# Performance work log

Measured on AMD Instinct MI355X. Metric: run time of the kernel, lower is better.

Reference implementation:

```python
import jax, jax.numpy as jnp
import numpy as np

B, S, D, H, FF = 2, 2048, 1024, 16, 4096
DK = D // H
LOCAL_WINDOW, STRIDE = 128, 128
NEG = -1000000000.0
EPS = 1e-5


def _layernorm(x, g, b):
    mu = jnp.mean(x, axis=-1, keepdims=True)
    var = jnp.mean(jnp.square(x - mu), axis=-1, keepdims=True)
    return (x - mu) * jax.lax.rsqrt(var + EPS) * g + b


def _strided_mask(seq):
    # allowed(i, j): j <= i and (i-j <= local_window or (i-j) % stride == 0)
    i = jnp.arange(seq)[:, None]
    j = jnp.arange(seq)[None, :]
    d = i - j
    return (d >= 0) & ((d <= LOCAL_WINDOW) | (d % STRIDE == 0))  # [S, S] bool


def setup_inputs() -> dict:
    key = jax.random.key(0)
    ks = jax.random.split(key, 18)
    w = lambda k, shape: jax.random.normal(k, shape, jnp.float32) * 0.02
    return {
        "x": jax.random.normal(ks[0], (B, S, D), jnp.float32),
        "mask": jnp.ones((1, 1, S, S), jnp.int32),
        "Wq": w(ks[1], (D, D)), "bq": jnp.zeros((D,), jnp.float32),
        "Wk": w(ks[2], (D, D)), "bk": jnp.zeros((D,), jnp.float32),
        "Wv": w(ks[3], (D, D)), "bv": jnp.zeros((D,), jnp.float32),
        "Wo": w(ks[4], (D, D)), "bo": jnp.zeros((D,), jnp.float32),
        "W1": w(ks[5], (D, FF)), "bf1": jnp.zeros((FF,), jnp.float32),
        "W2": w(ks[6], (FF, D)), "bf2": jnp.zeros((D,), jnp.float32),
        "g1": jnp.ones((D,), jnp.float32), "bl1": jnp.zeros((D,), jnp.float32),
        "g2": jnp.ones((D,), jnp.float32), "bl2": jnp.zeros((D,), jnp.float32),
    }


def reference(x, mask, Wq, bq, Wk, bk, Wv, bv, Wo, bo,
              W1, bf1, W2, bf2, g1, bl1, g2, bl2):
    b, s, d = x.shape
    sm = _strided_mask(s)[None, None]  # [1,1,S,S]

    # pre-LN self-attention
    n = _layernorm(x, g1, bl1)
    split = lambda t: t.reshape(b, s, H, DK).transpose(0, 2, 1, 3)  # [B,H,S,DK]
    q = split(n @ Wq + bq)
    k = split(n @ Wk + bk)
    v = split(n @ Wv + bv)

    scores = jnp.einsum('bhqd,bhkd->bhqk', q, k) / jnp.sqrt(jnp.float32(DK))
    scores = jnp.where(sm, scores, NEG)          # strided/local mask
    scores = jnp.where(mask == 0, NEG, scores)   # user mask
    attn = jax.nn.softmax(scores, axis=-1)
    o = jnp.einsum('bhqk,bhkd->bhqd', attn, v)
    o = o.transpose(0, 2, 1, 3).reshape(b, s, d) @ Wo + bo
    x = x + o

    # pre-LN FFN (GELU exact, matching torch nn.GELU default)
    n2 = _layernorm(x, g2, bl2)
    ff = jax.nn.gelu(n2 @ W1 + bf1, approximate=False) @ W2 + bf2
    return x + ff
```

## Files before the change

### kernel.cpp

```cpp
#include <hip/hip_runtime.h>
#include <math.h>

typedef unsigned int u32;
typedef unsigned short u16;

#define B_  2
#define S_  2048
#define D_  1024
#define H_  16
#define DK_ 64
#define FF_ 4096
#define NEG_ -1000000000.0f

typedef __attribute__((ext_vector_type(8))) short short8;
typedef __attribute__((ext_vector_type(4))) float floatx4;
typedef __attribute__((ext_vector_type(4))) unsigned short ushort4_t;

__device__ inline u16 f2b(float f) {
    union { float f; u32 u; } v; v.f = f;
    u32 r = (v.u + 0x7fffu + ((v.u >> 16) & 1u)) >> 16;
    return (u16)r;
}
__device__ inline float b2f(u16 b) {
    union { u32 u; float f; } v; v.u = ((u32)b) << 16;
    return v.f;
}

__device__ inline void gl_lds16(const u16* g, u16* l) {
    __builtin_amdgcn_global_load_lds((const __attribute__((address_space(1))) u32*)g,
                                     (__attribute__((address_space(3))) u32*)l, 16, 0, 0);
}

__global__ void tconv4(const float* __restrict__ W0, const float* __restrict__ W1_,
                       const float* __restrict__ W2_, const float* __restrict__ W3,
                       u16* __restrict__ dstBase) {
    __shared__ float tile[32][33];
    int z = blockIdx.z;
    const float* Wm = (z == 0) ? W0 : (z == 1) ? W1_ : (z == 2) ? W2_ : W3;
    u16* Wt = dstBase + (size_t)z * 1024 * 1024;
    const int K = 1024, N = 1024;
    int n0 = blockIdx.x * 32, k0 = blockIdx.y * 32;
    int tx = threadIdx.x & 31, ty = threadIdx.x >> 5;
#pragma unroll
    for (int r = 0; r < 32; r += 8)
        tile[ty + r][tx] = Wm[(size_t)(k0 + ty + r) * N + n0 + tx];
    __syncthreads();
#pragma unroll
    for (int r = 0; r < 32; r += 8)
        Wt[(size_t)(n0 + ty + r) * K + k0 + tx] = f2b(tile[tx][ty + r]);
}

__global__ void tconv(const float* __restrict__ Wm, u16* __restrict__ Wt, int K, int N) {
    __shared__ float tile[32][33];
    int n0 = blockIdx.x * 32, k0 = blockIdx.y * 32;
    int tx = threadIdx.x & 31, ty = threadIdx.x >> 5;
#pragma unroll
    for (int r = 0; r < 32; r += 8)
        tile[ty + r][tx] = Wm[(size_t)(k0 + ty + r) * N + n0 + tx];
    __syncthreads();
#pragma unroll
    for (int r = 0; r < 32; r += 8)
        Wt[(size_t)(n0 + ty + r) * K + k0 + tx] = f2b(tile[tx][ty + r]);
}

__global__ void catbias(const float* __restrict__ bq, const float* __restrict__ bk,
                        const float* __restrict__ bv, float* __restrict__ out) {
    int i = blockIdx.x * 256 + threadIdx.x;
    float v = (i < 1024) ? bq[i] : (i < 2048) ? bk[i - 1024] : bv[i - 2048];
    out[i] = v;
}

__global__ __launch_bounds__(256)
void mask_tiles(const int* __restrict__ mask, int* __restrict__ tflag) {
    int jt = blockIdx.x, it = blockIdx.y;
    const int* base = mask + (size_t)it * 128 * S_ + jt * 128;
    int t = threadIdx.x;
    int ok = 1;
    for (int e = t; e < 128 * 32; e += 256) {
        int r = e >> 5, c4 = e & 31;
        int4 vv = *(const int4*)&base[(size_t)r * S_ + c4 * 4];
        ok &= (vv.x != 0) & (vv.y != 0) & (vv.z != 0) & (vv.w != 0);
    }
    ok = (int)__all(ok);
    __shared__ int red[4];
    if ((t & 63) == 0) red[t >> 6] = ok;
    __syncthreads();
    if (t == 0) tflag[it * 16 + jt] = red[0] & red[1] & red[2] & red[3];
}

__global__ __launch_bounds__(256)
void ln_bf16(const float* __restrict__ x, const float* __restrict__ g,
             const float* __restrict__ b, u16* __restrict__ out) {
    int row = blockIdx.x, t = threadIdx.x;
    int lane = t & 63, w = t >> 6;
    const float* xr = x + (size_t)row * D_;
    __shared__ float red[8];
    int col0 = t * 4;
    float4 xv = *(const float4*)&xr[col0];
    float v0 = xv.x, v1 = xv.y, v2 = xv.z, v3 = xv.w;
    float s = v0 + v1 + v2 + v3;
    s += __shfl_xor(s, 1); s += __shfl_xor(s, 2); s += __shfl_xor(s, 4);
    s += __shfl_xor(s, 8); s += __shfl_xor(s, 16); s += __shfl_xor(s, 32);
    if (lane == 0) red[w] = s;
    __syncthreads();
    float mu = (red[0] + red[1] + red[2] + red[3]) * (1.0f / D_);
    float d0 = v0 - mu, d1 = v1 - mu, d2 = v2 - mu, d3 = v3 - mu;
    float vs = d0 * d0 + d1 * d1 + d2 * d2 + d3 * d3;
    vs += __shfl_xor(vs, 1); vs += __shfl_xor(vs, 2); vs += __shfl_xor(vs, 4);
    vs += __shfl_xor(vs, 8); vs += __shfl_xor(vs, 16); vs += __shfl_xor(vs, 32);
    if (lane == 0) red[4 + w] = vs;
    __syncthreads();
    float rstd = rsqrtf((red[4] + red[5] + red[6] + red[7]) * (1.0f / D_) + 1e-5f);
    float4 gv = *(const float4*)&g[col0];
    float4 bv = *(const float4*)&b[col0];
    ushort4_t o;
    o[0] = f2b(d0 * rstd * gv.x + bv.x);
    o[1] = f2b(d1 * rstd * gv.y + bv.y);
    o[2] = f2b(d2 * rstd * gv.z + bv.z);
    o[3] = f2b(d3 * rstd * gv.w + bv.w);
    *(ushort4_t*)&out[(size_t)row * D_ + col0] = o;
}

__global__ __launch_bounds__(256)
void merge_ln(const u16* __restrict__ P, const float* __restrict__ x,
              const float* __restrict__ bo, const float* __restrict__ g,
              const float* __restrict__ bl, float* __restrict__ x1,
              u16* __restrict__ n2) {
    const size_t MN = (size_t)B_ * S_ * D_;
    int row = blockIdx.x, t = threadIdx.x;
    int lane = t & 63, w = t >> 6;
    size_t base = (size_t)row * D_;
    __shared__ float red[8];
    int col0 = t * 4;
    float4 xv = *(const float4*)&x[base + col0];
    float4 bv = *(const float4*)&bo[col0];
    ushort4_t p0 = *(const ushort4_t*)&P[base + col0];
    ushort4_t p1 = *(const ushort4_t*)&P[MN + base + col0];
    float v0 = xv.x + bv.x + b2f(p0[0]) + b2f(p1[0]);
    float v1 = xv.y + bv.y + b2f(p0[1]) + b2f(p1[1]);
    float v2 = xv.z + bv.z + b2f(p0[2]) + b2f(p1[2]);
    float v3 = xv.w + bv.w + b2f(p0[3]) + b2f(p1[3]);
    float s = v0 + v1 + v2 + v3;
    s += __shfl_xor(s, 1); s += __shfl_xor(s, 2); s += __shfl_xor(s, 4);
    s += __shfl_xor(s, 8); s += __shfl_xor(s, 16); s += __shfl_xor(s, 32);
    if (lane == 0) red[w] = s;
    __syncthreads();
    float mu = (red[0] + red[1] + red[2] + red[3]) * (1.0f / D_);
    float d0 = v0 - mu, d1 = v1 - mu, d2 = v2 - mu, d3 = v3 - mu;
    float vs = d0 * d0 + d1 * d1 + d2 * d2 + d3 * d3;
    vs += __shfl_xor(vs, 1); vs += __shfl_xor(vs, 2); vs += __shfl_xor(vs, 4);
    vs += __shfl_xor(vs, 8); vs += __shfl_xor(vs, 16); vs += __shfl_xor(vs, 32);
    if (lane == 0) red[4 + w] = vs;
    __syncthreads();
    float rstd = rsqrtf((red[4] + red[5] + red[6] + red[7]) * (1.0f / D_) + 1e-5f);
    float4 gv = *(const float4*)&g[col0];
    float4 blv = *(const float4*)&bl[col0];
    *(float4*)&x1[base + col0] = (float4){v0, v1, v2, v3};
    ushort4_t o;
    o[0] = f2b(d0 * rstd * gv.x + blv.x);
    o[1] = f2b(d1 * rstd * gv.y + blv.y);
    o[2] = f2b(d2 * rstd * gv.z + blv.z);
    o[3] = f2b(d3 * rstd * gv.w + blv.w);
    *(ushort4_t*)&n2[base + col0] = o;
}

#define BARR asm volatile("s_barrier" ::: "memory")

template <int EPI>
__global__ __launch_bounds__(512, 2)
void gemm8(const u16* __restrict__ A, const u16* __restrict__ Bt,
           const float* __restrict__ bias, void* __restrict__ Cv,
           int M, int N, int K, int ldA, int ldB) {
    __shared__ u16 sh2[65536];
    const int tid = threadIdx.x;
    const int lane = tid & 63, w = tid >> 6;
    const int wm = w >> 2, wn = w & 3;
    const int c = lane & 15, g = lane >> 4;
    const int cbase = c * 128 + g * 16;
    const int xo = (c & 7) << 4;

    int nMt = gridDim.x;
    int nwg = gridDim.x * gridDim.y;
    int id = blockIdx.x + nMt * blockIdx.y;
    int qq = nwg >> 3;
    int sid = (id & 7) * qq + (id >> 3);
    int m0 = (sid % nMt) * 256, n0 = (sid / nMt) * 256;
    size_t koff = (size_t)blockIdx.z * K;

    const int nT = K >> 6, nI = nT >> 1;

    const int sr = tid >> 3;
    const int sk = ((tid & 7) * 8) ^ (((tid >> 3) & 7) << 3);
    const u16* gA0 = A + (size_t)(m0 + sr) * ldA + koff + sk;
    const u16* gB0 = Bt + (size_t)(n0 + sr) * ldB + koff + sk;
    const int dst0 = w * 512;

#define STG_A(t_, h_) do { \
    const u16* s_ = gA0 + (size_t)(h_) * 128 * ldA + (t_) * 64; \
    u16* l_ = &sh2[((((t_) & 1) * 2 + (h_)) * 8192) + dst0]; \
    gl_lds16(s_, l_); \
    gl_lds16(s_ + (size_t)64 * ldA, l_ + 4096); \
} while (0)
#define STG_B(t_, h_) do { \
    const u16* s_ = gB0 + (size_t)(h_) * 128 * ldB + (t_) * 64; \
    u16* l_ = &sh2[32768 + ((((t_) & 1) * 2 + (h_)) * 8192) + dst0]; \
    gl_lds16(s_, l_); \
    gl_lds16(s_ + (size_t)64 * ldB, l_ + 4096); \
} while (0)

    short8 fa[8], fb0[4], fb1[4];
    floatx4 acc[2][2][4][2];
#pragma unroll
    for (int i = 0; i < 2; i++)
#pragma unroll
        for (int j = 0; j < 2; j++)
#pragma unroll
            for (int a = 0; a < 4; a++)
#pragma unroll
                for (int b2 = 0; b2 < 2; b2++)
                    acc[i][j][a][b2] = (floatx4){0.f, 0.f, 0.f, 0.f};

#define DS_A(d_, qr_) do { \
    int rb_ = ((d_) * 2 + wm) * 16384; \
    _Pragma("unroll") for (int a_ = 0; a_ < 4; a_++) \
    _Pragma("unroll") for (int k_ = 0; k_ < 2; k_++) { \
        int lin_ = (qr_) * 8192 + a_ * 2048 + cbase + k_ * 64; \
        fa[a_ * 2 + k_] = *(const short8*)((const char*)sh2 + rb_ + (lin_ ^ xo)); } \
} while (0)
#define DS_B(d_, qc_, fb_) do { \
    int rb_ = 65536 + ((d_) * 2 + (wn >> 1)) * 16384; \
    _Pragma("unroll") for (int b_ = 0; b_ < 2; b_++) \
    _Pragma("unroll") for (int k_ = 0; k_ < 2; k_++) { \
        int lin_ = (wn & 1) * 8192 + (qc_) * 4096 + b_ * 2048 + cbase + k_ * 64; \
        fb_[b_ * 2 + k_] = *(const short8*)((const char*)sh2 + rb_ + (lin_ ^ xo)); } \
} while (0)
#define MFMA16(qr_, qc_, fb_) do { \
    __builtin_amdgcn_s_setprio(1); \
    _Pragma("unroll") for (int a_ = 0; a_ < 4; a_++) \
    _Pragma("unroll") for (int b_ = 0; b_ < 2; b_++) \
    _Pragma("unroll") for (int k_ = 0; k_ < 2; k_++) \
        acc[qr_][qc_][a_][b_] = __builtin_amdgcn_mfma_f32_16x16x32_bf16( \
            fa[a_ * 2 + k_], fb_[b_ * 2 + k_], acc[qr_][qc_][a_][b_], 0, 0, 0); \
    __builtin_amdgcn_s_setprio(0); \
} while (0)

    STG_B(0, 0); STG_B(0, 1); STG_A(0, 0); STG_A(0, 1);
    STG_A(1, 0); STG_A(1, 1);
    asm volatile("s_waitcnt vmcnt(4)" ::: "memory");
    BARR;

    for (int it2 = 0; it2 < nI; it2++) {
        const int t1 = 2 * it2 + 1, tn0 = t1 + 1, tn1 = t1 + 2;
        DS_A(0, 0); DS_B(0, 0, fb0);
        STG_B(t1, 0);
        MFMA16(0, 0, fb0); BARR;
        DS_B(0, 1, fb1);
        STG_B(t1, 1);
        MFMA16(0, 1, fb1); BARR;
        DS_A(0, 1);
        if (tn0 < nT) STG_B(tn0, 0);
        MFMA16(1, 1, fb1); BARR;
        if (tn0 < nT) {
            STG_B(tn0, 1);
            asm volatile("s_waitcnt vmcnt(4)" ::: "memory");
        } else {
            asm volatile("s_waitcnt vmcnt(0)" ::: "memory");
        }
        MFMA16(1, 0, fb0); BARR;
        DS_A(1, 0); DS_B(1, 0, fb0);
        if (tn0 < nT) STG_A(tn0, 0);
        MFMA16(0, 0, fb0); BARR;
        DS_B(1, 1, fb1);
        if (tn0 < nT) STG_A(tn0, 1);
        MFMA16(0, 1, fb1); BARR;
        DS_A(1, 1);
        if (tn1 < nT) STG_A(tn1, 0);
        MFMA16(1, 1, fb1); BARR;
        if (tn1 < nT) STG_A(tn1, 1);
        if (it2 + 1 < nI) asm volatile("s_waitcnt vmcnt(4)" ::: "memory");
        MFMA16(1, 0, fb0); BARR;
    }

#pragma unroll
    for (int qr = 0; qr < 2; qr++)
#pragma unroll
        for (int qc = 0; qc < 2; qc++)
#pragma unroll
            for (int a = 0; a < 4; a++)
#pragma unroll
                for (int b2 = 0; b2 < 2; b2++) {
                    int mrow = m0 + wm * 128 + qr * 64 + a * 16 + g * 4;
                    int ncol = n0 + wn * 64 + qc * 32 + b2 * 16 + c;
                    float bv = (EPI == 3) ? 0.f : bias[ncol];
#pragma unroll
                    for (int r = 0; r < 4; r++) {
                        int m = mrow + r;
                        float vvv = acc[qr][qc][a][b2][r] + bv;
                        if (EPI == 0) {
                            int which = ncol >> 10, col = ncol & 1023;
                            if (which == 0) vvv *= 0.125f;
                            int bb = m >> 11, ss = m & 2047, hh = col >> 6, dk = col & 63;
                            ((u16*)Cv)[(size_t)which * ((size_t)B_ * S_ * D_) +
                                       ((((size_t)bb * H_ + hh) * S_) + ss) * DK_ + dk] = f2b(vvv);
                        } else if (EPI == 2) {
                            float u = 0.79788456080286536f * fmaf(0.044715f * vvv, vvv * vvv, vvv);
                            float th = 1.f - 2.f / (1.f + __expf(2.f * u));
                            ((u16*)Cv)[(size_t)m * N + ncol] = f2b(0.5f * vvv * (1.f + th));
                        } else {
                            ((u16*)Cv)[(size_t)blockIdx.z * M * N + (size_t)m * N + ncol] = f2b(vvv);
                        }
                    }
                }
#undef STG_A
#undef STG_B
#undef DS_A
#undef DS_B
#undef MFMA16
}

__global__ __launch_bounds__(256)
void ffn2_merge(const u16* __restrict__ P, const float* __restrict__ x1,
                const float* __restrict__ bf2, float* __restrict__ out) {
    const size_t MN = (size_t)B_ * S_ * D_;
    int e = (blockIdx.x * 256 + threadIdx.x) * 4;
    float4 xv = *(const float4*)&x1[e];
    float4 bv = *(const float4*)&bf2[e & 1023];
    float o0 = xv.x + bv.x, o1 = xv.y + bv.y, o2 = xv.z + bv.z, o3 = xv.w + bv.w;
#pragma unroll
    for (int z = 0; z < 4; z++) {
        ushort4_t pv = *(const ushort4_t*)&P[z * MN + e];
        o0 += b2f(pv[0]); o1 += b2f(pv[1]); o2 += b2f(pv[2]); o3 += b2f(pv[3]);
    }
    *(float4*)&out[e] = (float4){o0, o1, o2, o3};
}

#define MAXB_ 14
__global__ __launch_bounds__(256)
void attn4(const u16* __restrict__ q, const u16* __restrict__ k,
           const u16* __restrict__ v, const int* __restrict__ mask,
           const int* __restrict__ tileOK, u16* __restrict__ ob) {
    __shared__ u16 sh[19456];
    u16* Kw = sh;
    u16* Qs = sh + 13824;
    u16* Vh = sh + 12800;

    const int bh = blockIdx.x;
    const int i0 = (31 - blockIdx.y) * 64;
    const int b  = bh >> 4, h = bh & 15;
    const int t  = threadIdx.x;
    const int lane = t & 63, w = t >> 6;
    const int c = lane & 15, g = lane >> 4;
    const int g4 = g * 4;
    const int qloc16 = w * 16;

    const u16* qg = q + ((size_t)bh * S_ + i0) * DK_;
    const u16* kg = k + (size_t)bh * S_ * DK_;
    const u16* vg = v + (size_t)bh * S_ * DK_;

    const int wlo = (i0 >= 128) ? i0 - 128 : 0;
    const int wn  = i0 + 64 - wlo;
    const int nb  = (i0 >= 256) ? (i0 >> 7) - 1 : 0;
    const int jb0 = i0 & 127;
    const int dd0 = i0 - wlo;

    bool allOK = true;
    {
        const int* rowf = tileOK + (i0 >> 7) * 16;
        int jt0 = wlo >> 7, jt1 = (i0 + 63) >> 7;
        for (int jt = jt0; jt <= jt1; jt++) allOK &= (rowf[jt] != 0);
        for (int m = 0; m < nb; m++) allOK &= (rowf[m] != 0);
    }

    for (int e = t; e < 64 * 8; e += 256) {
        int row = e >> 3, dc = e & 7;
        *(short8*)&Qs[row * 72 + dc * 8] = *(const short8*)(qg + row * 64 + dc * 8);
    }
    for (int e = t; e < wn * 8; e += 256) {
        int row = e >> 3, dc = e & 7;
        *(short8*)&Kw[row * 72 + dc * 8] = *(const short8*)(kg + (size_t)(wlo + row) * 64 + dc * 8);
    }
    __syncthreads();

    float sbr[MAXB_];
    {
        short8 qv0 = *(const short8*)&Qs[(qloc16 + c) * 72 + g * 8];
        short8 qv1 = *(const short8*)&Qs[(qloc16 + c) * 72 + 32 + g * 8];
#pragma unroll
        for (int m = 0; m < MAXB_; m++) {
            sbr[m] = NEG_;
            if (m < nb) {
                int jrow = jb0 + (m << 7) + qloc16 + c;
                short8 kv0 = *(const short8*)(kg + (size_t)jrow * 64 + g * 8);
                short8 kv1 = *(const short8*)(kg + (size_t)jrow * 64 + 32 + g * 8);
                float p = 0.f;
#pragma unroll
                for (int i = 0; i < 8; i++) {
                    p += b2f((u16)qv0[i]) * b2f((u16)kv0[i]);
                    p += b2f((u16)qv1[i]) * b2f((u16)kv1[i]);
                }
                p += __shfl_xor(p, 16);
                p += __shfl_xor(p, 32);
                if (!allOK && mask[(size_t)(i0 + qloc16 + c) * S_ + jrow] == 0) p = NEG_;
                sbr[m] = p;
            }
        }
    }

    floatx4 sc[12];
#pragma unroll
    for (int ct = 0; ct < 12; ct++) sc[ct] = (floatx4){0.f, 0.f, 0.f, 0.f};
    {
        short8 fa0 = *(const short8*)&Qs[(qloc16 + c) * 72 + g * 8];
        short8 fa1 = *(const short8*)&Qs[(qloc16 + c) * 72 + 32 + g * 8];
#pragma unroll
        for (int ct = 0; ct < 12; ct++) {
            short8 fb0 = *(const short8*)&Kw[(ct * 16 + c) * 72 + g * 8];
            short8 fb1 = *(const short8*)&Kw[(ct * 16 + c) * 72 + 32 + g * 8];
            sc[ct] = __builtin_amdgcn_mfma_f32_16x16x32_bf16(fa0, fb0, sc[ct], 0, 0, 0);
            sc[ct] = __builtin_amdgcn_mfma_f32_16x16x32_bf16(fa1, fb1, sc[ct], 0, 0, 0);
        }
    }

#pragma unroll
    for (int ct = 0; ct < 12; ct++) {
        int cidx = ct * 16 + c;
        int j = wlo + cidx;
#pragma unroll
        for (int r = 0; r < 4; r++) {
            int qloc = qloc16 + g4 + r;
            int d = dd0 + qloc - cidx;
            bool ok = (d >= 0) && (d <= 128);
            if (ok && !allOK) ok = (mask[(size_t)(i0 + qloc) * S_ + j] != 0);
            sc[ct][r] = ok ? sc[ct][r] : NEG_;
        }
    }

    float mv[4], inv[4];
#pragma unroll
    for (int r = 0; r < 4; r++) {
        float bs[MAXB_];
#pragma unroll
        for (int m = 0; m < MAXB_; m++)
            bs[m] = (m < nb) ? __shfl(sbr[m], g4 + r, 64) : NEG_;
        float mm = -1e30f;
#pragma unroll
        for (int ct = 0; ct < 12; ct++) mm = fmaxf(mm, sc[ct][r]);
        mm = fmaxf(mm, __shfl_xor(mm, 1));
        mm = fmaxf(mm, __shfl_xor(mm, 2));
        mm = fmaxf(mm, __shfl_xor(mm, 4));
        mm = fmaxf(mm, __shfl_xor(mm, 8));
#pragma unroll
        for (int m = 0; m < MAXB_; m++)
            if (m < nb) mm = fmaxf(mm, bs[m]);
        float sum = 0.f;
#pragma unroll
        for (int ct = 0; ct < 12; ct++) {
            float e = __expf(sc[ct][r] - mm);
            sc[ct][r] = e;
            sum += e;
        }
        sum += __shfl_xor(sum, 1);
        sum += __shfl_xor(sum, 2);
        sum += __shfl_xor(sum, 4);
        sum += __shfl_xor(sum, 8);
#pragma unroll
        for (int m = 0; m < MAXB_; m++)
            if (m < nb) sum += __expf(bs[m] - mm);
        mv[r] = mm;
        inv[r] = 1.f / sum;
    }

    __syncthreads();
    u16* P = Kw;
#pragma unroll
    for (int ct = 0; ct < 12; ct++)
#pragma unroll
        for (int r = 0; r < 4; r++)
            P[(qloc16 + g4 + r) * 200 + ct * 16 + c] = f2b(sc[ct][r]);

    for (int e = t; e < 768; e += 256) {
        int dc = e / 96, jl = e - dc * 96;
        short8 val = {0, 0, 0, 0, 0, 0, 0, 0};
        if (jl < wn) val = *(const short8*)(vg + (size_t)(wlo + jl) * 64 + dc * 8);
#pragma unroll
        for (int i = 0; i < 8; i++) Vh[(dc * 8 + i) * 104 + jl] = (u16)val[i];
    }
    __syncthreads();

    floatx4 o[4];
#pragma unroll
    for (int nt = 0; nt < 4; nt++) o[nt] = (floatx4){0.f, 0.f, 0.f, 0.f};
#pragma unroll
    for (int ks = 0; ks < 3; ks++) {
        short8 pa = *(const short8*)&P[(qloc16 + c) * 200 + ks * 32 + g * 8];
#pragma unroll
        for (int nt = 0; nt < 4; nt++) {
            short8 vb = *(const short8*)&Vh[(nt * 16 + c) * 104 + ks * 32 + g * 8];
            o[nt] = __builtin_amdgcn_mfma_f32_16x16x32_bf16(pa, vb, o[nt], 0, 0, 0);
        }
    }

    if (wn > 96) {
        __syncthreads();
        for (int e = t; e < 768; e += 256) {
            int dc = e / 96, jl = e - dc * 96;
            int j2 = 96 + jl;
            short8 val = {0, 0, 0, 0, 0, 0, 0, 0};
            if (j2 < wn) val = *(const short8*)(vg + (size_t)(wlo + j2) * 64 + dc * 8);
#pragma unroll
            for (int i = 0; i < 8; i++) Vh[(dc * 8 + i) * 104 + jl] = (u16)val[i];
        }
        __syncthreads();
#pragma unroll
        for (int ks = 0; ks < 3; ks++) {
            short8 pa = *(const short8*)&P[(qloc16 + c) * 200 + 96 + ks * 32 + g * 8];
#pragma unroll
            for (int nt = 0; nt < 4; nt++) {
                short8 vb = *(const short8*)&Vh[(nt * 16 + c) * 104 + ks * 32 + g * 8];
                o[nt] = __builtin_amdgcn_mfma_f32_16x16x32_bf16(pa, vb, o[nt], 0, 0, 0);
            }
        }
    }

#pragma unroll
    for (int m = 0; m < MAXB_; m++) {
        if (m < nb) {
            int vbase = jb0 + (m << 7) + qloc16 + g4;
            u16 vv[4][4];
#pragma unroll
            for (int r = 0; r < 4; r++)
#pragma unroll
                for (int nt = 0; nt < 4; nt++)
                    vv[r][nt] = vg[(size_t)(vbase + r) * 64 + nt * 16 + c];
#pragma unroll
            for (int r = 0; r < 4; r++) {
                float bs = __shfl(sbr[m], g4 + r, 64);
                float pb = __expf(bs - mv[r]);
#pragma unroll
                for (int nt = 0; nt < 4; nt++)
                    o[nt][r] += pb * b2f(vv[r][nt]);
            }
        }
    }

#pragma unroll
    for (int nt = 0; nt < 4; nt++) {
#pragma unroll
        for (int r = 0; r < 4; r++) {
            int qi = i0 + qloc16 + g4 + r;
            ob[((size_t)b * S_ + qi) * D_ + h * 64 + nt * 16 + c] = f2b(o[nt][r] * inv[r]);
        }
    }
}

extern "C" void kernel_launch(void* const* d_in, const int* in_sizes, int n_in,
                              void* d_out, int out_size, void* d_ws, size_t ws_size,
                              hipStream_t stream) {
    const float* x    = (const float*)d_in[0];
    const int*   mask = (const int*)  d_in[1];
    const float* Wq   = (const float*)d_in[2];
    const float* bq   = (const float*)d_in[3];
    const float* Wk   = (const float*)d_in[4];
    const float* bk   = (const float*)d_in[5];
    const float* Wv   = (const float*)d_in[6];
    const float* bv   = (const float*)d_in[7];
    const float* Wo   = (const float*)d_in[8];
    const float* bo   = (const float*)d_in[9];
    const float* W1   = (const float*)d_in[10];
    const float* bf1  = (const float*)d_in[11];
    const float* W2   = (const float*)d_in[12];
    const float* bf2  = (const float*)d_in[13];
    const float* g1   = (const float*)d_in[14];
    const float* bl1  = (const float*)d_in[15];
    const float* g2   = (const float*)d_in[16];
    const float* bl2  = (const float*)d_in[17];

    char* wsb = (char*)d_ws;
    const size_t MB = 1024 * 1024;
    u16*   WtQKV  = (u16*)(wsb + 0);
    u16*   WtO    = (u16*)(wsb + 6 * MB);
    u16*   Wt1    = (u16*)(wsb + 8 * MB);
    u16*   Wt2    = (u16*)(wsb + 16 * MB);
    u16*   n1b    = (u16*)(wsb + 24 * MB);
    u16*   qkv    = (u16*)(wsb + 32 * MB);
    u16*   obb    = (u16*)(wsb + 56 * MB);
    float* x1     = (float*)(wsb + 32 * MB);
    u16*   ff1b   = (u16*)(wsb + 48 * MB);
    u16*   Ppart  = (u16*)(wsb + 82 * MB);
    u16*   PpartO = (u16*)(wsb + 82 * MB);
    float* bcat   = (float*)(wsb + 114 * MB);
    int*   tflag  = (int*)(wsb + 115 * MB);
    u16*   n2b    = n1b;

    const int M = B_ * S_;
    const size_t SZ = (size_t)B_ * S_ * D_;

    mask_tiles<<<dim3(16, 16), 256, 0, stream>>>(mask, tflag);
    tconv4<<<dim3(32, 32, 4), 256, 0, stream>>>(Wq, Wk, Wv, Wo, WtQKV);
    tconv<<<dim3(128, 32), 256, 0, stream>>>(W1, Wt1, 1024, 4096);
    tconv<<<dim3(32, 128), 256, 0, stream>>>(W2, Wt2, 4096, 1024);
    catbias<<<12, 256, 0, stream>>>(bq, bk, bv, bcat);

    ln_bf16<<<M, 256, 0, stream>>>(x, g1, bl1, n1b);

    gemm8<0><<<dim3(16, 12, 1), 512, 0, stream>>>(n1b, WtQKV, bcat, qkv,
                                                  M, 3072, 1024, 1024, 1024);

    attn4<<<dim3(32, 32), 256, 0, stream>>>(qkv, qkv + SZ, qkv + 2 * SZ, mask, tflag, obb);

    gemm8<3><<<dim3(16, 4, 2), 512, 0, stream>>>(obb, WtO, nullptr, PpartO,
                                                 M, 1024, 512, 1024, 1024);
    merge_ln<<<M, 256, 0, stream>>>(PpartO, x, bo, g2, bl2, x1, n2b);

    gemm8<2><<<dim3(16, 16, 1), 512, 0, stream>>>(n2b, Wt1, bf1, ff1b,
                                                  M, 4096, 1024, 1024, 1024);

    gemm8<3><<<dim3(16, 4, 4), 512, 0, stream>>>(ff1b, Wt2, nullptr, Ppart,
                                                 M, 1024, 1024, 4096, 4096);
    ffn2_merge<<<(int)(SZ / 1024), 256, 0, stream>>>(Ppart, x1, bf2, (float*)d_out);
}
```

Measured before the change: 365.1 us.

## Add 128x128 double-buffered GEMM for QKV, O-proj and FFN2 with fewer splits

Adds a new 256-thread GEMM kernel that uses 128x128 tiles, 32-wide K steps and double-buffered LDS loaded directly from global memory. It replaces the larger 512-thread gemm8 for the QKV projection, the output projection and FFN2. FFN2 now splits K two ways instead of four, so the merge kernel reads only two partial buffers. The goal is higher occupancy, more workgroups in flight and less partial-sum traffic. The cost is smaller tiles with less data reuse, and a shallower pipeline than gemm8 had.

```diff
diff --git a/kernel.cpp b/kernel.cpp
--- a/kernel.cpp
+++ b/kernel.cpp
@@ -164,6 +164,101 @@
     *(ushort4_t*)&n2[base + col0] = o;
 }
 
+template <int EPI>
+__global__ __launch_bounds__(256, 4)
+void gemm_bt(const u16* __restrict__ A, const u16* __restrict__ Bt,
+             const float* __restrict__ bias, const float* __restrict__ R,
+             void* __restrict__ Cv, int M, int N, int K, int ldA, int ldB) {
+    __shared__ u16 As[2][128 * 32];
+    __shared__ u16 Bs[2][128 * 32];
+    int tid = threadIdx.x;
+    int lane = tid & 63, w = tid >> 6;
+    int wm = w >> 1, wn = w & 1;
+    int nMt = gridDim.x, nwg = gridDim.x * gridDim.y;
+    int id = blockIdx.x + nMt * blockIdx.y;
+    int qq = nwg >> 3;
+    int sid = (id & 7) * qq + (id >> 3);
+    int m0 = (sid % nMt) * 128, n0 = (sid / nMt) * 128;
+    size_t koff = (size_t)blockIdx.z * K;
+
+    floatx4 acc[4][4];
+#pragma unroll
+    for (int a = 0; a < 4; a++)
+#pragma unroll
+        for (int b2 = 0; b2 < 4; b2++) acc[a][b2] = (floatx4){0.f, 0.f, 0.f, 0.f};
+
+    int r4 = lane >> 2;
+    int qg = ((lane & 3) ^ ((lane >> 3) & 3)) * 8;
+    const u16* Ag0 = A + (size_t)(m0 + w * 16 + r4) * ldA + koff + qg;
+    const u16* Bg0 = Bt + (size_t)(n0 + w * 16 + r4) * ldB + koff + qg;
+    const int ldsOff = (w * 16) * 32;
+
+    int c = lane & 15, g = lane >> 4;
+    int sw = (g ^ ((c >> 1) & 3)) * 8;
+
+    const int nIter = K >> 5;
+
+    gl_lds16(Ag0, &As[0][ldsOff]);
+    gl_lds16(Ag0 + (size_t)64 * ldA, &As[0][ldsOff + 64 * 32]);
+    gl_lds16(Bg0, &Bs[0][ldsOff]);
+    gl_lds16(Bg0 + (size_t)64 * ldB, &Bs[0][ldsOff + 64 * 32]);
+
+    for (int it = 0; it < nIter; it++) {
+        __syncthreads();
+        int cur = it & 1, nxt = cur ^ 1;
+        if (it + 1 < nIter) {
+            int kk = (it + 1) << 5;
+            gl_lds16(Ag0 + kk, &As[nxt][ldsOff]);
+            gl_lds16(Ag0 + kk + (size_t)64 * ldA, &As[nxt][ldsOff + 64 * 32]);
+            gl_lds16(Bg0 + kk, &Bs[nxt][ldsOff]);
+            gl_lds16(Bg0 + kk + (size_t)64 * ldB, &Bs[nxt][ldsOff + 64 * 32]);
+        }
+        short8 fa[4], fb[4];
+#pragma unroll
+        for (int a = 0; a < 4; a++)
+            fa[a] = *(const short8*)&As[cur][(wm * 64 + a * 16 + c) * 32 + sw];
+#pragma unroll
+        for (int b2 = 0; b2 < 4; b2++)
+            fb[b2] = *(const short8*)&Bs[cur][(wn * 64 + b2 * 16 + c) * 32 + sw];
+#pragma unroll
+        for (int a = 0; a < 4; a++)
+#pragma unroll
+            for (int b2 = 0; b2 < 4; b2++)
+                acc[a][b2] = __builtin_amdgcn_mfma_f32_16x16x32_bf16(fa[a], fb[b2], acc[a][b2], 0, 0, 0);
+    }
+
+    int mb = m0 + wm * 64, nb = n0 + wn * 64;
+#pragma unroll
+    for (int a = 0; a < 4; a++) {
+#pragma unroll
+        for (int b2 = 0; b2 < 4; b2++) {
+            int mrow = mb + a * 16 + g * 4;
+            int ncol = nb + b2 * 16 + c;
+            float bv = (EPI == 3) ? 0.f : bias[ncol];
+#pragma unroll
+            for (int r = 0; r < 4; r++) {
+                int m = mrow + r;
+                float vvv = acc[a][b2][r] + bv;
+                if (EPI == 0) {
+                    int which = ncol >> 10, col = ncol & 1023;
+                    if (which == 0) vvv *= 0.125f;
+                    int bb = m >> 11, ss = m & 2047, hh = col >> 6, dk = col & 63;
+                    ((u16*)Cv)[(size_t)which * ((size_t)B_ * S_ * D_) +
+                               ((((size_t)bb * H_ + hh) * S_) + ss) * DK_ + dk] = f2b(vvv);
+                } else if (EPI == 1) {
+                    ((float*)Cv)[(size_t)m * N + ncol] = vvv + R[(size_t)m * N + ncol];
+                } else if (EPI == 2) {
+                    float u = 0.79788456080286536f * fmaf(0.044715f * vvv, vvv * vvv, vvv);
+                    float th = 1.f - 2.f / (1.f + __expf(2.f * u));
+                    ((u16*)Cv)[(size_t)m * N + ncol] = f2b(0.5f * vvv * (1.f + th));
+                } else {
+                    ((u16*)Cv)[(size_t)blockIdx.z * M * N + (size_t)m * N + ncol] = f2b(vvv);
+                }
+            }
+        }
+    }
+}
+
 #define BARR asm volatile("s_barrier" ::: "memory")
 
 template <int EPI>
@@ -318,6 +413,7 @@
 #undef MFMA16
 }
 
+template <int NP>
 __global__ __launch_bounds__(256)
 void ffn2_merge(const u16* __restrict__ P, const float* __restrict__ x1,
                 const float* __restrict__ bf2, float* __restrict__ out) {
@@ -327,7 +423,7 @@
     float4 bv = *(const float4*)&bf2[e & 1023];
     float o0 = xv.x + bv.x, o1 = xv.y + bv.y, o2 = xv.z + bv.z, o3 = xv.w + bv.w;
 #pragma unroll
-    for (int z = 0; z < 4; z++) {
+    for (int z = 0; z < NP; z++) {
         ushort4_t pv = *(const ushort4_t*)&P[z * MN + e];
         o0 += b2f(pv[0]); o1 += b2f(pv[1]); o2 += b2f(pv[2]); o3 += b2f(pv[3]);
     }
@@ -603,19 +699,19 @@
 
     ln_bf16<<<M, 256, 0, stream>>>(x, g1, bl1, n1b);
 
-    gemm8<0><<<dim3(16, 12, 1), 512, 0, stream>>>(n1b, WtQKV, bcat, qkv,
-                                                  M, 3072, 1024, 1024, 1024);
+    gemm_bt<0><<<dim3(32, 24), 256, 0, stream>>>(n1b, WtQKV, bcat, nullptr, qkv,
+                                                 M, 3072, 1024, 1024, 1024);
 
     attn4<<<dim3(32, 32), 256, 0, stream>>>(qkv, qkv + SZ, qkv + 2 * SZ, mask, tflag, obb);
 
-    gemm8<3><<<dim3(16, 4, 2), 512, 0, stream>>>(obb, WtO, nullptr, PpartO,
-                                                 M, 1024, 512, 1024, 1024);
+    gemm_bt<3><<<dim3(32, 8, 2), 256, 0, stream>>>(obb, WtO, nullptr, nullptr, PpartO,
+                                                   M, 1024, 512, 1024, 1024);
     merge_ln<<<M, 256, 0, stream>>>(PpartO, x, bo, g2, bl2, x1, n2b);
 
     gemm8<2><<<dim3(16, 16, 1), 512, 0, stream>>>(n2b, Wt1, bf1, ff1b,
                                                   M, 4096, 1024, 1024, 1024);
 
-    gemm8<3><<<dim3(16, 4, 4), 512, 0, stream>>>(ff1b, Wt2, nullptr, Ppart,
-                                                 M, 1024, 1024, 4096, 4096);
-    ffn2_merge<<<(int)(SZ / 1024), 256, 0, stream>>>(Ppart, x1, bf2, (float*)d_out);
-}
+    gemm_bt<3><<<dim3(32, 8, 2), 256, 0, stream>>>(ff1b, Wt2, nullptr, nullptr, Ppart,
+                                                   M, 1024, 2048, 4096, 4096);
+    ffn2_merge<2><<<(int)(SZ / 1024), 256, 0, stream>>>(Ppart, x1, bf2, (float*)d_out);
+}
```

Measured after the change: 369.5 us. About the same (+1.2%).
